# Performance work log

Hardware: AMD Instinct MI355X
Metric: run time of the kernel (lower is better)

## Reference

```python
import jax, jax.numpy as jnp
import numpy as np

K = 6                 # color-coding parameter; K-1 message-passing steps
N = 50000             # num nodes
E = 1600000           # num edges (avg degree 32)
F = 384               # num_node_features = K * 2**K


def setup_inputs() -> dict:
    key = jax.random.key(0)
    k1, k2, k3, k4, k5 = jax.random.split(key, 5)
    s = 1.0 / np.sqrt(F)
    x = jax.random.normal(k1, (N, F), dtype=jnp.float32)
    edge_index = jax.random.randint(k2, (2, E), 0, N, dtype=jnp.int32)
    batch = jnp.zeros((N,), dtype=jnp.int32)  # unused by forward, kept for signature parity
    W_rel = jax.random.normal(k3, (F, F), dtype=jnp.float32) * s   # GraphConv lin_rel weight
    W_root = jax.random.normal(k4, (F, F), dtype=jnp.float32) * s  # GraphConv lin_root weight
    W_lin = jax.random.normal(k5, (1, F), dtype=jnp.float32) * s   # readout linear (no bias)
    return {"x": x, "edge_index": edge_index, "batch": batch,
            "W_rel": W_rel, "W_root": W_root, "W_lin": W_lin}


def reference(x, edge_index, batch, W_rel, W_root, W_lin):
    src = edge_index[0]
    dst = edge_index[1]
    # K-1 iterations of PyG GraphConv(aggr='add', bias=False) + relu:
    #   out = segment_sum(x[src] -> dst) @ W_rel^T + x @ W_root^T
    for _ in range(K - 1):
        agg = jax.ops.segment_sum(x[src], dst, num_segments=N)  # [N, F]
        x = jax.nn.relu(agg @ W_rel.T + x @ W_root.T)
    # readout: Linear(F, 1, bias=False)
    return x @ W_lin.T  # [N, 1]
```

## Files before the change

kernel.cpp:

```cpp
#include <hip/hip_runtime.h>
#include <hip/hip_bf16.h>

#define NN 50000
#define EE 1600000
#define FF 384
#define MPAD 50048
#define NITER 5

typedef unsigned int u32;
typedef unsigned short u16;
typedef __attribute__((ext_vector_type(8))) short short8;
typedef __attribute__((ext_vector_type(4))) float f32x4;

typedef const __attribute__((address_space(1))) void* gptr_t;
typedef __attribute__((address_space(3))) void* lptr_t;

__device__ __forceinline__ float bf_lo(u32 u) {
  u32 v = u << 16;
  return __builtin_bit_cast(float, v);
}
__device__ __forceinline__ float bf_hi(u32 u) {
  u32 v = u & 0xFFFF0000u;
  return __builtin_bit_cast(float, v);
}
__device__ __forceinline__ u32 f2bf(float f) {
  u32 u = __builtin_bit_cast(u32, f);
  return (u + 0x7FFFu + ((u >> 16) & 1u)) >> 16;
}
__device__ __forceinline__ u32 pack2(float lo, float hi) {
  return f2bf(lo) | (f2bf(hi) << 16);
}
__device__ __forceinline__ void load16_lds(const void* g, void* l) {
  __builtin_amdgcn_global_load_lds((gptr_t)g, (lptr_t)l, 16, 0, 0);
}

__global__ void hist_kernel(const int* __restrict__ key, int* __restrict__ cnt) {
  int e = blockIdx.x * 256 + threadIdx.x;
  if (e < EE) atomicAdd(&cnt[key[e]], 1);
}

__global__ void scan_kernel(const int* __restrict__ cnt, int* __restrict__ row_start,
                            int* __restrict__ cursor) {
  __shared__ int wsum[4];
  const int CH = 196;
  int t = threadIdx.x;
  int lo = t * CH;
  int hi = lo + CH; if (hi > NN) hi = NN;
  int s = 0;
  int n4 = (hi - lo) >> 2;
  const int4* p = (const int4*)(cnt + lo);
  for (int i = 0; i < n4; ++i) { int4 c = p[i]; s += c.x + c.y + c.z + c.w; }
  int lane = t & 63, w = t >> 6;
  int v = s;
  for (int d = 1; d < 64; d <<= 1) { int u = __shfl_up(v, d, 64); if (lane >= d) v += u; }
  if (lane == 63) wsum[w] = v;
  __syncthreads();
  int run = v - s;
  for (int i = 0; i < w; ++i) run += wsum[i];
  int4* q1 = (int4*)(row_start + lo);
  int4* q2 = (int4*)(cursor + lo);
  for (int k = 0; k < n4; ++k) {
    int4 c = p[k];
    int4 o; o.x = run; o.y = run + c.x; o.z = o.y + c.y; o.w = o.z + c.z;
    run = o.w + c.w;
    q1[k] = o; q2[k] = o;
  }
  if (hi == NN && lo < NN) row_start[NN] = run;
}

__global__ void scatter_kernel(const int* __restrict__ src, const int* __restrict__ dst,
                               int* __restrict__ cursor, int* __restrict__ col) {
  int e = blockIdx.x * 256 + threadIdx.x;
  if (e < EE) {
    int d = dst[e];
    int p = atomicAdd(&cursor[d], 1);
    col[p] = src[e];
  }
}

__global__ void convert_x_kernel(const float* __restrict__ xin, u16* __restrict__ xout) {
  size_t i = ((size_t)blockIdx.x * 256 + threadIdx.x) * 4;
  if (i >= (size_t)NN * FF) return;
  float4 f = *(const float4*)(xin + i);
  u32 o0 = pack2(f.x, f.y);
  u32 o1 = pack2(f.z, f.w);
  u32* q = (u32*)(xout + i);
  q[0] = o0; q[1] = o1;
}

__global__ void build_bt_kernel(const float* __restrict__ Wr, const float* __restrict__ Wt,
                                u16* __restrict__ Bt) {
  int i = blockIdx.x * 256 + threadIdx.x;
  if (i >= FF * 2 * FF) return;
  int n = i / (2 * FF);
  int k = i - n * (2 * FF);
  float v = (k < FF) ? Wr[n * FF + k] : Wt[n * FF + (k - FF)];
  Bt[i] = (u16)f2bf(v);
}

struct u32x3 { u32 x, y, z; };
#define ACC6(u)                                  \
  a0 += bf_lo(u.x); a1 += bf_hi(u.x);            \
  a2 += bf_lo(u.y); a3 += bf_hi(u.y);            \
  a4 += bf_lo(u.z); a5 += bf_hi(u.z);

__global__ void spmm_kernel(const u16* __restrict__ x, const int* __restrict__ rs,
                            const int* __restrict__ col, u16* __restrict__ agg) {
  int row = blockIdx.x * 4 + (threadIdx.x >> 6);
  int lane = threadIdx.x & 63;
  if (row >= NN) return;
  int j0 = rs[row], j1 = rs[row + 1];
  float a0 = 0.f, a1 = 0.f, a2 = 0.f, a3 = 0.f, a4 = 0.f, a5 = 0.f;
  const int off = lane * 3;
  int j = j0;
  for (; j + 4 <= j1; j += 4) {
    int s0 = col[j], s1 = col[j + 1], s2 = col[j + 2], s3 = col[j + 3];
    u32x3 u0 = *(const u32x3*)((const u32*)(x + (size_t)s0 * FF) + off);
    u32x3 u1 = *(const u32x3*)((const u32*)(x + (size_t)s1 * FF) + off);
    u32x3 u2 = *(const u32x3*)((const u32*)(x + (size_t)s2 * FF) + off);
    u32x3 u3 = *(const u32x3*)((const u32*)(x + (size_t)s3 * FF) + off);
    ACC6(u0); ACC6(u1); ACC6(u2); ACC6(u3);
  }
  for (; j < j1; ++j) {
    int s0 = col[j];
    u32x3 u0 = *(const u32x3*)((const u32*)(x + (size_t)s0 * FF) + off);
    ACC6(u0);
  }
  u32* q = (u32*)(agg + (size_t)row * FF) + off;
  q[0] = pack2(a0, a1);
  q[1] = pack2(a2, a3);
  q[2] = pack2(a4, a5);
}

__global__ __launch_bounds__(256) void gemm_kernel(
    const u16* __restrict__ Aagg, const u16* __restrict__ Ax,
    const u16* __restrict__ Bt, u16* __restrict__ Xout) {
  __shared__ __align__(16) u16 As[2][128 * 64];
  __shared__ __align__(16) u16 Bs[2][128 * 64];

  const int orig = blockIdx.x;
  const int xcd = orig & 7, idx = orig >> 3;
  const int base = (xcd < 5) ? xcd * 147 : 5 * 147 + (xcd - 5) * 146;
  const int wg = base + idx;
  const int m0 = (wg / 3) * 128;
  const int n0 = (wg % 3) * 128;

  const int tid = threadIdx.x;
  const int lane = tid & 63;
  const int w = tid >> 6;
  const int wr = w >> 1, wc = w & 1;

  const int sr = lane >> 3;
  const int sbc = (lane & 7) << 4;

  f32x4 acc[4][4] = {};

#define STAGE(KT, BUF)                                                          \
  {                                                                             \
    const u16* Asrc_ = ((KT) < 6) ? Aagg : Ax;                                  \
    const int kbA_ = (((KT) < 6) ? (KT) : (KT)-6) << 7;                         \
    const int kbB_ = (KT) << 7;                                                 \
    _Pragma("unroll")                                                           \
    for (int i = 0; i < 4; ++i) {                                               \
      const int r = w * 32 + i * 8 + sr;                                        \
      const int swz = sbc ^ ((r & 7) << 4);                                     \
      load16_lds((const char*)Asrc_ + (size_t)(m0 + r) * 768 + kbA_ + swz,      \
                 &As[BUF][(w * 32 + i * 8) * 64]);                              \
      load16_lds((const char*)Bt + (size_t)(n0 + r) * 1536 + kbB_ + swz,        \
                 &Bs[BUF][(w * 32 + i * 8) * 64]);                              \
    }                                                                           \
  }

  STAGE(0, 0);
  __syncthreads();

  int buf = 0;
  for (int kt = 0; kt < 12; ++kt) {
    if (kt < 11) STAGE(kt + 1, buf ^ 1);
#pragma unroll
    for (int ks = 0; ks < 2; ++ks) {
      short8 af[4], bfm[4];
#pragma unroll
      for (int mi = 0; mi < 4; ++mi) {
        const int r = wr * 64 + mi * 16 + (lane & 15);
        const int bc = (ks * 64 + ((lane >> 4) << 4)) ^ ((r & 7) << 4);
        af[mi] = *(const short8*)((const char*)&As[buf][0] + r * 128 + bc);
      }
#pragma unroll
      for (int ni = 0; ni < 4; ++ni) {
        const int r = wc * 64 + ni * 16 + (lane & 15);
        const int bc = (ks * 64 + ((lane >> 4) << 4)) ^ ((r & 7) << 4);
        bfm[ni] = *(const short8*)((const char*)&Bs[buf][0] + r * 128 + bc);
      }
#pragma unroll
      for (int mi = 0; mi < 4; ++mi)
#pragma unroll
        for (int ni = 0; ni < 4; ++ni)
          acc[mi][ni] = __builtin_amdgcn_mfma_f32_16x16x32_bf16(af[mi], bfm[ni], acc[mi][ni], 0, 0, 0);
    }
    __syncthreads();
    buf ^= 1;
  }

#pragma unroll
  for (int mi = 0; mi < 4; ++mi) {
#pragma unroll
    for (int r = 0; r < 4; ++r) {
      const int row = m0 + wr * 64 + mi * 16 + ((lane >> 4) << 2) + r;
      u16* orow = Xout + (size_t)row * FF + n0 + wc * 64 + (lane & 15);
#pragma unroll
      for (int ni = 0; ni < 4; ++ni) {
        float v = fmaxf(acc[mi][ni][r], 0.0f);
        orow[ni * 16] = (u16)f2bf(v);
      }
    }
  }
#undef STAGE
}

__global__ void readout_kernel(const u16* __restrict__ x, const float* __restrict__ wl,
                               float* __restrict__ out) {
  int row = blockIdx.x * 4 + (threadIdx.x >> 6);
  int lane = threadIdx.x & 63;
  if (row >= NN) return;
  const u32* p = (const u32*)(x + (size_t)row * FF) + lane * 3;
  u32 u0 = p[0], u1 = p[1], u2 = p[2];
  const float* w = wl + lane * 6;
  float s = bf_lo(u0) * w[0] + bf_hi(u0) * w[1] +
            bf_lo(u1) * w[2] + bf_hi(u1) * w[3] +
            bf_lo(u2) * w[4] + bf_hi(u2) * w[5];
#pragma unroll
  for (int off = 32; off > 0; off >>= 1) s += __shfl_down(s, off, 64);
  if (lane == 0) out[row] = s;
}

extern "C" void kernel_launch(void* const* d_in, const int* in_sizes, int n_in,
                              void* d_out, int out_size, void* d_ws, size_t ws_size,
                              hipStream_t stream) {
  const float* x_in = (const float*)d_in[0];
  const int* ei = (const int*)d_in[1];
  const float* W_rel = (const float*)d_in[3];
  const float* W_root = (const float*)d_in[4];
  const float* W_lin = (const float*)d_in[5];
  float* out = (float*)d_out;

  char* ws = (char*)d_ws;
  int* cnt = (int*)(ws);
  int* row_start = (int*)(ws + 200064);
  int* cursor = (int*)(ws + 400128);
  int* col = (int*)(ws + 600192);
  u16* Bt = (u16*)(ws + 7000192);
  u16* agg = (u16*)(ws + 7590016);
  u16* x0 = (u16*)(ws + 46026880);
  u16* x1 = (u16*)(ws + 84463744);
  if (ws_size < (size_t)122900608) return;

  const int* esrc = ei;
  const int* edst = ei + EE;

  hipMemsetAsync(cnt, 0, NN * sizeof(int), stream);
  hipMemsetAsync(agg + (size_t)NN * FF, 0, (size_t)(MPAD - NN) * FF * sizeof(u16), stream);
  hipMemsetAsync(x0 + (size_t)NN * FF, 0, (size_t)(MPAD - NN) * FF * sizeof(u16), stream);
  hipMemsetAsync(x1 + (size_t)NN * FF, 0, (size_t)(MPAD - NN) * FF * sizeof(u16), stream);

  hist_kernel<<<EE / 256, 256, 0, stream>>>(edst, cnt);
  scan_kernel<<<1, 256, 0, stream>>>(cnt, row_start, cursor);
  scatter_kernel<<<EE / 256, 256, 0, stream>>>(esrc, edst, cursor, col);
  convert_x_kernel<<<(NN * FF / 4 + 255) / 256, 256, 0, stream>>>(x_in, x0);
  build_bt_kernel<<<(FF * 2 * FF + 255) / 256, 256, 0, stream>>>(W_rel, W_root, Bt);

  u16* xs = x0;
  u16* xd = x1;
  for (int t = 0; t < NITER; ++t) {
    spmm_kernel<<<NN / 4, 256, 0, stream>>>(xs, row_start, col, agg);
    gemm_kernel<<<(MPAD / 128) * (FF / 128), 256, 0, stream>>>(agg, xs, Bt, xd);
    u16* tmp = xs; xs = xd; xd = tmp;
  }
  readout_kernel<<<NN / 4, 256, 0, stream>>>(xs, W_lin, out);
}
```

Baseline: 1.291 ms.

## Cover full N per GEMM block and read B fragments directly from global

The GEMM now gives each 512-thread block a 128-row tile covering all 384 output columns, so the A tile is loaded into LDS once instead of three times. B fragments are read straight from global memory (expected to hit in cache) instead of being staged in LDS, and the LDS B buffers are removed. The XCD remapping and launch grid are adjusted to match. The SpMM inner loop also drops from 4-edge to 2-edge unrolling with scalar u32 loads. The risks are global-load latency for B inside the MFMA loop and lower memory-level parallelism in the SpMM.

```diff
diff --git a/kernel.cpp b/kernel.cpp
--- a/kernel.cpp
+++ b/kernel.cpp
@@ -98,12 +98,6 @@
   Bt[i] = (u16)f2bf(v);
 }
 
-struct u32x3 { u32 x, y, z; };
-#define ACC6(u)                                  \
-  a0 += bf_lo(u.x); a1 += bf_hi(u.x);            \
-  a2 += bf_lo(u.y); a3 += bf_hi(u.y);            \
-  a4 += bf_lo(u.z); a5 += bf_hi(u.z);
-
 __global__ void spmm_kernel(const u16* __restrict__ x, const int* __restrict__ rs,
                             const int* __restrict__ col, u16* __restrict__ agg) {
   int row = blockIdx.x * 4 + (threadIdx.x >> 6);
@@ -111,63 +105,64 @@
   if (row >= NN) return;
   int j0 = rs[row], j1 = rs[row + 1];
   float a0 = 0.f, a1 = 0.f, a2 = 0.f, a3 = 0.f, a4 = 0.f, a5 = 0.f;
-  const int off = lane * 3;
   int j = j0;
-  for (; j + 4 <= j1; j += 4) {
-    int s0 = col[j], s1 = col[j + 1], s2 = col[j + 2], s3 = col[j + 3];
-    u32x3 u0 = *(const u32x3*)((const u32*)(x + (size_t)s0 * FF) + off);
-    u32x3 u1 = *(const u32x3*)((const u32*)(x + (size_t)s1 * FF) + off);
-    u32x3 u2 = *(const u32x3*)((const u32*)(x + (size_t)s2 * FF) + off);
-    u32x3 u3 = *(const u32x3*)((const u32*)(x + (size_t)s3 * FF) + off);
-    ACC6(u0); ACC6(u1); ACC6(u2); ACC6(u3);
-  }
-  for (; j < j1; ++j) {
+  for (; j + 2 <= j1; j += 2) {
+    int s0 = col[j], s1 = col[j + 1];
+    const u32* p0 = (const u32*)(x + (size_t)s0 * FF) + lane * 3;
+    const u32* p1 = (const u32*)(x + (size_t)s1 * FF) + lane * 3;
+    u32 u0 = p0[0], u1 = p0[1], u2 = p0[2];
+    u32 v0 = p1[0], v1 = p1[1], v2 = p1[2];
+    a0 += bf_lo(u0); a1 += bf_hi(u0);
+    a2 += bf_lo(u1); a3 += bf_hi(u1);
+    a4 += bf_lo(u2); a5 += bf_hi(u2);
+    a0 += bf_lo(v0); a1 += bf_hi(v0);
+    a2 += bf_lo(v1); a3 += bf_hi(v1);
+    a4 += bf_lo(v2); a5 += bf_hi(v2);
+  }
+  if (j < j1) {
     int s0 = col[j];
-    u32x3 u0 = *(const u32x3*)((const u32*)(x + (size_t)s0 * FF) + off);
-    ACC6(u0);
-  }
-  u32* q = (u32*)(agg + (size_t)row * FF) + off;
+    const u32* p0 = (const u32*)(x + (size_t)s0 * FF) + lane * 3;
+    u32 u0 = p0[0], u1 = p0[1], u2 = p0[2];
+    a0 += bf_lo(u0); a1 += bf_hi(u0);
+    a2 += bf_lo(u1); a3 += bf_hi(u1);
+    a4 += bf_lo(u2); a5 += bf_hi(u2);
+  }
+  u32* q = (u32*)(agg + (size_t)row * FF) + lane * 3;
   q[0] = pack2(a0, a1);
   q[1] = pack2(a2, a3);
   q[2] = pack2(a4, a5);
 }
 
-__global__ __launch_bounds__(256) void gemm_kernel(
+__global__ __launch_bounds__(512, 2) void gemm_kernel(
     const u16* __restrict__ Aagg, const u16* __restrict__ Ax,
     const u16* __restrict__ Bt, u16* __restrict__ Xout) {
   __shared__ __align__(16) u16 As[2][128 * 64];
-  __shared__ __align__(16) u16 Bs[2][128 * 64];
 
   const int orig = blockIdx.x;
   const int xcd = orig & 7, idx = orig >> 3;
-  const int base = (xcd < 5) ? xcd * 147 : 5 * 147 + (xcd - 5) * 146;
-  const int wg = base + idx;
-  const int m0 = (wg / 3) * 128;
-  const int n0 = (wg % 3) * 128;
+  const int wg = ((xcd < 7) ? xcd * 49 : 7 * 49 + (xcd - 7) * 48) + idx;
+  const int m0 = wg * 128;
 
   const int tid = threadIdx.x;
   const int lane = tid & 63;
   const int w = tid >> 6;
-  const int wr = w >> 1, wc = w & 1;
-
-  const int sr = lane >> 3;
-  const int sbc = (lane & 7) << 4;
-
-  f32x4 acc[4][4] = {};
+  const int wr = w >> 2;
+  const int wc = w & 3;
+
+  f32x4 acc[4][6] = {};
 
 #define STAGE(KT, BUF)                                                          \
   {                                                                             \
     const u16* Asrc_ = ((KT) < 6) ? Aagg : Ax;                                  \
     const int kbA_ = (((KT) < 6) ? (KT) : (KT)-6) << 7;                         \
-    const int kbB_ = (KT) << 7;                                                 \
     _Pragma("unroll")                                                           \
-    for (int i = 0; i < 4; ++i) {                                               \
-      const int r = w * 32 + i * 8 + sr;                                        \
-      const int swz = sbc ^ ((r & 7) << 4);                                     \
+    for (int i = 0; i < 2; ++i) {                                               \
+      const int c = tid + i * 512;                                              \
+      const int r = c >> 3;                                                     \
+      const int bc = (c & 7) << 4;                                              \
+      const int swz = bc ^ ((r & 7) << 4);                                      \
       load16_lds((const char*)Asrc_ + (size_t)(m0 + r) * 768 + kbA_ + swz,      \
-                 &As[BUF][(w * 32 + i * 8) * 64]);                              \
-      load16_lds((const char*)Bt + (size_t)(n0 + r) * 1536 + kbB_ + swz,        \
-                 &Bs[BUF][(w * 32 + i * 8) * 64]);                              \
+                 (char*)&As[BUF][0] + c * 16);                                  \
     }                                                                           \
   }
 
@@ -177,9 +172,16 @@
   int buf = 0;
   for (int kt = 0; kt < 12; ++kt) {
     if (kt < 11) STAGE(kt + 1, buf ^ 1);
+    const int kbB = kt << 7;
 #pragma unroll
     for (int ks = 0; ks < 2; ++ks) {
-      short8 af[4], bfm[4];
+      short8 af[4], bfm[6];
+#pragma unroll
+      for (int ni = 0; ni < 6; ++ni) {
+        const int n = wc * 96 + ni * 16 + (lane & 15);
+        bfm[ni] = *(const short8*)((const char*)Bt + (size_t)n * 1536 + kbB +
+                                   ks * 64 + ((lane >> 4) << 4));
+      }
 #pragma unroll
       for (int mi = 0; mi < 4; ++mi) {
         const int r = wr * 64 + mi * 16 + (lane & 15);
@@ -187,15 +189,9 @@
         af[mi] = *(const short8*)((const char*)&As[buf][0] + r * 128 + bc);
       }
 #pragma unroll
-      for (int ni = 0; ni < 4; ++ni) {
-        const int r = wc * 64 + ni * 16 + (lane & 15);
-        const int bc = (ks * 64 + ((lane >> 4) << 4)) ^ ((r & 7) << 4);
-        bfm[ni] = *(const short8*)((const char*)&Bs[buf][0] + r * 128 + bc);
-      }
-#pragma unroll
       for (int mi = 0; mi < 4; ++mi)
 #pragma unroll
-        for (int ni = 0; ni < 4; ++ni)
+        for (int ni = 0; ni < 6; ++ni)
           acc[mi][ni] = __builtin_amdgcn_mfma_f32_16x16x32_bf16(af[mi], bfm[ni], acc[mi][ni], 0, 0, 0);
     }
     __syncthreads();
@@ -207,9 +203,9 @@
 #pragma unroll
     for (int r = 0; r < 4; ++r) {
       const int row = m0 + wr * 64 + mi * 16 + ((lane >> 4) << 2) + r;
-      u16* orow = Xout + (size_t)row * FF + n0 + wc * 64 + (lane & 15);
-#pragma unroll
-      for (int ni = 0; ni < 4; ++ni) {
+      u16* orow = Xout + (size_t)row * FF + wc * 96 + (lane & 15);
+#pragma unroll
+      for (int ni = 0; ni < 6; ++ni) {
         float v = fmaxf(acc[mi][ni][r], 0.0f);
         orow[ni * 16] = (u16)f2bf(v);
       }
@@ -273,7 +269,7 @@
   u16* xd = x1;
   for (int t = 0; t < NITER; ++t) {
     spmm_kernel<<<NN / 4, 256, 0, stream>>>(xs, row_start, col, agg);
-    gemm_kernel<<<(MPAD / 128) * (FF / 128), 256, 0, stream>>>(agg, xs, Bt, xd);
+    gemm_kernel<<<MPAD / 128, 512, 0, stream>>>(agg, xs, Bt, xd);
     u16* tmp = xs; xs = xd; xd = tmp;
   }
   readout_kernel<<<NN / 4, 256, 0, stream>>>(xs, W_lin, out);
```

Result: slower. 1.466 ms (+13.5%).
